# Kernel optimization log

Measured on AMD Instinct MI355X. Metric: run time of the kernel, lower is better.

Reference implementation:

```python
import jax, jax.numpy as jnp
import numpy as np


def setup_inputs() -> dict:
    key = jax.random.key(0)
    k1, k2 = jax.random.split(key)
    n, c, h, w = 32, 256, 64, 64
    x = jax.random.normal(k1, (n, c, h, w), dtype=jnp.float32)
    tau = jax.random.uniform(k2, (), dtype=jnp.float32)  # blend factor in (0,1)
    return {"x": x, "tau": tau, "topk_keep_num": 409}


def reference(x, tau, topk_keep_num):
    # x: [n, c, h, w]; keep top-k |x| entries over the flattened h*w axis per (n, c).
    n, c, h, w = x.shape
    hw = h * w
    if topk_keep_num == hw:
        return x
    xr = x.reshape(n, c, hw)
    # top-k indices by absolute value along last axis
    _, idx = jax.lax.top_k(jnp.abs(xr), topk_keep_num)  # idx: [n, c, k]
    # scatter ones at selected positions (torch.zeros_like(...).scatter_(2, idx, 1))
    bi = jnp.arange(n)[:, None, None]
    ci = jnp.arange(c)[None, :, None]
    mask = jnp.zeros_like(xr).at[bi, ci, idx].set(1.0)
    sparse_x = (mask * xr).reshape(n, c, h, w)
    # blend: sparse_x * tau + x * (1 - tau)  (tau == 1.0 reduces to sparse_x)
    return sparse_x * tau + x * (1.0 - tau)
```

## Files before the change

### kernel.cpp

```cpp
#include <hip/hip_runtime.h>
#include <hip/hip_bf16.h>

#define TPB 256
#define HW 4096

typedef unsigned int uint32;

template<int NB>
__device__ inline void find_crossing(uint32* hist, uint32* chunkSum, uint32 kk,
                                     uint32* sh_bin, uint32* sh_rank)
{
    const int tid = threadIdx.x;
    constexpr int CH = NB / TPB;
    uint32 s = 0;
#pragma unroll
    for (int j = 0; j < CH; ++j) s += hist[tid * CH + j];
    chunkSum[tid] = s;
    __syncthreads();
    if (tid < 64) {
        uint32 g = 0;
#pragma unroll
        for (int j = 0; j < 4; ++j) g += chunkSum[tid * 4 + j];
        uint32 suf = g;
#pragma unroll
        for (int d = 1; d < 64; d <<= 1) {
            uint32 v = __shfl_down(suf, d, 64);
            suf += (tid + d < 64) ? v : 0u;
        }
        unsigned long long m = __ballot(suf >= kk);
        int lstar = 63 - __clzll(m);
        uint32 cumAbove = (lstar < 63) ? __shfl(suf, lstar + 1, 64) : 0u;
        if (tid == lstar) {
            uint32 c = cumAbove;
            int bin = lstar * 4 * CH;
            uint32 rank = 1;
            bool done = false;
            for (int cc = lstar * 4 + 3; cc >= lstar * 4 && !done; --cc) {
                uint32 cs = chunkSum[cc];
                if (c + cs >= kk) {
                    for (int b = cc * CH + CH - 1; b >= cc * CH; --b) {
                        uint32 h = hist[b];
                        if (c + h >= kk) { bin = b; rank = kk - c; break; }
                        c += h;
                    }
                    done = true;
                } else {
                    c += cs;
                }
            }
            *sh_bin = (uint32)bin;
            *sh_rank = rank;
        }
    }
    __syncthreads();
}

__global__ void __launch_bounds__(TPB)
topk_blend_kernel(const float* __restrict__ x, const float* __restrict__ taup,
                  const int* __restrict__ kp, float* __restrict__ out, int nrows)
{
    __shared__ uint32 hist[2048];
    __shared__ uint32 chunkSum[TPB];
    __shared__ uint32 sh_bin, sh_rank, sh_cnt, sh_idxcut;

    const int tid = threadIdx.x;
    const int row = blockIdx.x;
    if (row >= nrows) return;

    const float4* xr  = reinterpret_cast<const float4*>(x + (size_t)row * HW);
    float4*       orw = reinterpret_cast<float4*>(out + (size_t)row * HW);

    float4 v[4];
#pragma unroll
    for (int j = 0; j < 4; ++j) v[j] = xr[tid + j * TPB];

    const uint32 K  = (uint32)(*kp);
    const float tau = *taup;

#pragma unroll
    for (int j = 0; j < 8; ++j) hist[tid + j * TPB] = 0;
    if (tid == 0) { sh_cnt = 0; sh_idxcut = 0xFFFFFFFFu; }
    __syncthreads();

    uint32 key[16];
#pragma unroll
    for (int j = 0; j < 4; ++j) {
        const float* pv = reinterpret_cast<const float*>(&v[j]);
#pragma unroll
        for (int l = 0; l < 4; ++l)
            key[j * 4 + l] = __float_as_uint(pv[l]) & 0x7fffffffu;
    }

#pragma unroll
    for (int e = 0; e < 16; ++e) atomicAdd(&hist[key[e] >> 20], 1u);
    __syncthreads();
    find_crossing<2048>(hist, chunkSum, K, &sh_bin, &sh_rank);
    const uint32 b1 = sh_bin;
    const uint32 k1 = sh_rank;

#pragma unroll
    for (int j = 0; j < 8; ++j) hist[tid + j * TPB] = 0;
    __syncthreads();
#pragma unroll
    for (int e = 0; e < 16; ++e)
        if ((key[e] >> 20) == b1) atomicAdd(&hist[(key[e] >> 9) & 2047u], 1u);
    __syncthreads();
    find_crossing<2048>(hist, chunkSum, k1, &sh_bin, &sh_rank);
    const uint32 b2 = sh_bin;
    const uint32 k2 = sh_rank;
    const uint32 p2 = (b1 << 11) | b2;

#pragma unroll
    for (int j = 0; j < 2; ++j) hist[tid + j * TPB] = 0;
    __syncthreads();
#pragma unroll
    for (int e = 0; e < 16; ++e)
        if ((key[e] >> 9) == p2) atomicAdd(&hist[key[e] & 511u], 1u);
    __syncthreads();
    find_crossing<512>(hist, chunkSum, k2, &sh_bin, &sh_rank);
    const uint32 b3  = sh_bin;
    const uint32 k3  = sh_rank;
    const uint32 ceq = hist[b3];
    const uint32 t   = (p2 << 9) | b3;

    uint32 idx_cut = 0xFFFFFFFFu;
    if (k3 < ceq) {
        uint32* tied = hist;
        __syncthreads();
#pragma unroll
        for (int e = 0; e < 16; ++e) {
            if (key[e] == t) {
                uint32 pos = atomicAdd(&sh_cnt, 1u);
                if (pos < 2048u) {
                    int j = e >> 2, l = e & 3;
                    tied[pos] = (uint32)(4 * (j * TPB + tid) + l);
                }
            }
        }
        __syncthreads();
        uint32 c2 = min(sh_cnt, 2048u);
        for (uint32 i = tid; i < c2; i += TPB) {
            uint32 my = tied[i];
            uint32 r = 0;
            for (uint32 jj = 0; jj < c2; ++jj) r += (tied[jj] < my) ? 1u : 0u;
            if (r == k3 - 1u) sh_idxcut = my;
        }
        __syncthreads();
        idx_cut = sh_idxcut;
    }

    const float om = 1.0f - tau;
#pragma unroll
    for (int j = 0; j < 4; ++j) {
        float4 o;
        const float* pv = reinterpret_cast<const float*>(&v[j]);
        float* po = reinterpret_cast<float*>(&o);
#pragma unroll
        for (int l = 0; l < 4; ++l) {
            int e = j * 4 + l;
            uint32 kb = key[e];
            uint32 eidx = (uint32)(4 * (j * TPB + tid) + l);
            bool keep = (kb > t) || (kb == t && eidx <= idx_cut);
            float xv = pv[l];
            po[l] = keep ? (xv * tau + xv * om) : (xv * om);
        }
        orw[tid + j * TPB] = o;
    }
}

extern "C" void kernel_launch(void* const* d_in, const int* in_sizes, int n_in,
                              void* d_out, int out_size, void* d_ws, size_t ws_size,
                              hipStream_t stream)
{
    (void)n_in; (void)out_size; (void)d_ws; (void)ws_size;
    const float* x   = (const float*)d_in[0];
    const float* tau = (const float*)d_in[1];
    const int*   kp  = (const int*)d_in[2];
    float*       out = (float*)d_out;
    const int nrows  = in_sizes[0] / HW;
    topk_blend_kernel<<<nrows, TPB, 0, stream>>>(x, tau, kp, out, nrows);
}
```

Measured before the change: 230.6 us.

## Replace three-pass radix select with one wide histogram plus candidate ranking

The three-level radix select (2048/2048/512 bins, each with its own find-crossing pass) becomes a single 4096-bin histogram on the top 12 bits of |x|. The crossing bin comes from a wave-level suffix scan plus a per-thread scan over 16 register-held bins. Elements in that bin are compacted into shared memory with ballot-based wave aggregation, then ranked brute-force on packed (low mantissa, reversed index) keys to find the exact cutoff. This removes two histogram rounds and several barriers, but the quadratic candidate ranking could get expensive if many values land in one bin.

```diff
diff --git a/kernel.cpp b/kernel.cpp
--- a/kernel.cpp
+++ b/kernel.cpp
@@ -3,165 +3,156 @@
 
 #define TPB 256
 #define HW 4096
+#define NB 4096
 
-typedef unsigned int uint32;
-
-template<int NB>
-__device__ inline void find_crossing(uint32* hist, uint32* chunkSum, uint32 kk,
-                                     uint32* sh_bin, uint32* sh_rank)
-{
-    const int tid = threadIdx.x;
-    constexpr int CH = NB / TPB;
-    uint32 s = 0;
-#pragma unroll
-    for (int j = 0; j < CH; ++j) s += hist[tid * CH + j];
-    chunkSum[tid] = s;
-    __syncthreads();
-    if (tid < 64) {
-        uint32 g = 0;
-#pragma unroll
-        for (int j = 0; j < 4; ++j) g += chunkSum[tid * 4 + j];
-        uint32 suf = g;
-#pragma unroll
-        for (int d = 1; d < 64; d <<= 1) {
-            uint32 v = __shfl_down(suf, d, 64);
-            suf += (tid + d < 64) ? v : 0u;
-        }
-        unsigned long long m = __ballot(suf >= kk);
-        int lstar = 63 - __clzll(m);
-        uint32 cumAbove = (lstar < 63) ? __shfl(suf, lstar + 1, 64) : 0u;
-        if (tid == lstar) {
-            uint32 c = cumAbove;
-            int bin = lstar * 4 * CH;
-            uint32 rank = 1;
-            bool done = false;
-            for (int cc = lstar * 4 + 3; cc >= lstar * 4 && !done; --cc) {
-                uint32 cs = chunkSum[cc];
-                if (c + cs >= kk) {
-                    for (int b = cc * CH + CH - 1; b >= cc * CH; --b) {
-                        uint32 h = hist[b];
-                        if (c + h >= kk) { bin = b; rank = kk - c; break; }
-                        c += h;
-                    }
-                    done = true;
-                } else {
-                    c += cs;
-                }
-            }
-            *sh_bin = (uint32)bin;
-            *sh_rank = rank;
-        }
-    }
-    __syncthreads();
-}
+typedef unsigned int u32;
+typedef unsigned long long u64;
 
 __global__ void __launch_bounds__(TPB)
 topk_blend_kernel(const float* __restrict__ x, const float* __restrict__ taup,
-                  const int* __restrict__ kp, float* __restrict__ out, int nrows)
+                  const int* __restrict__ kp, float* __restrict__ out)
 {
-    __shared__ uint32 hist[2048];
-    __shared__ uint32 chunkSum[TPB];
-    __shared__ uint32 sh_bin, sh_rank, sh_cnt, sh_idxcut;
+    __shared__ u32 hist[NB];
+    __shared__ u32 waveTot[4];
+    __shared__ u32 sh_b, sh_k1, sh_cnt, sh_pstar;
 
-    const int tid = threadIdx.x;
-    const int row = blockIdx.x;
-    if (row >= nrows) return;
+    const int tid  = threadIdx.x;
+    const int lane = tid & 63;
+    const int wv   = tid >> 6;
+    const int row  = blockIdx.x;
 
     const float4* xr  = reinterpret_cast<const float4*>(x + (size_t)row * HW);
     float4*       orw = reinterpret_cast<float4*>(out + (size_t)row * HW);
 
-    float4 v[4];
+    uint4* h4 = reinterpret_cast<uint4*>(hist);
+    const uint4 z4 = make_uint4(0u, 0u, 0u, 0u);
 #pragma unroll
-    for (int j = 0; j < 4; ++j) v[j] = xr[tid + j * TPB];
+    for (int j = 0; j < NB / 4 / TPB; ++j) h4[tid + j * TPB] = z4;
+    if (tid == 0) sh_cnt = 0;
 
-    const uint32 K  = (uint32)(*kp);
+    u32 r[16];
+#pragma unroll
+    for (int j = 0; j < 4; ++j) {
+        float4 v = xr[tid + j * TPB];
+        r[4 * j + 0] = __float_as_uint(v.x);
+        r[4 * j + 1] = __float_as_uint(v.y);
+        r[4 * j + 2] = __float_as_uint(v.z);
+        r[4 * j + 3] = __float_as_uint(v.w);
+    }
+    const u32  K   = (u32)(*kp);
     const float tau = *taup;
-
-#pragma unroll
-    for (int j = 0; j < 8; ++j) hist[tid + j * TPB] = 0;
-    if (tid == 0) { sh_cnt = 0; sh_idxcut = 0xFFFFFFFFu; }
     __syncthreads();
 
-    uint32 key[16];
+    if (K >= HW) {
 #pragma unroll
-    for (int j = 0; j < 4; ++j) {
-        const float* pv = reinterpret_cast<const float*>(&v[j]);
-#pragma unroll
-        for (int l = 0; l < 4; ++l)
-            key[j * 4 + l] = __float_as_uint(pv[l]) & 0x7fffffffu;
+        for (int j = 0; j < 4; ++j) {
+            float4 o;
+            o.x = __uint_as_float(r[4 * j + 0]);
+            o.y = __uint_as_float(r[4 * j + 1]);
+            o.z = __uint_as_float(r[4 * j + 2]);
+            o.w = __uint_as_float(r[4 * j + 3]);
+            orw[tid + j * TPB] = o;
+        }
+        return;
     }
 
 #pragma unroll
-    for (int e = 0; e < 16; ++e) atomicAdd(&hist[key[e] >> 20], 1u);
+    for (int e = 0; e < 16; ++e)
+        atomicAdd(&hist[(r[e] & 0x7fffffffu) >> 19], 1u);
     __syncthreads();
-    find_crossing<2048>(hist, chunkSum, K, &sh_bin, &sh_rank);
-    const uint32 b1 = sh_bin;
-    const uint32 k1 = sh_rank;
 
+    u32 hh[16];
+    {
+        uint4 a0 = h4[tid * 4 + 0], a1 = h4[tid * 4 + 1];
+        uint4 a2 = h4[tid * 4 + 2], a3 = h4[tid * 4 + 3];
+        hh[0]=a0.x; hh[1]=a0.y; hh[2]=a0.z;  hh[3]=a0.w;
+        hh[4]=a1.x; hh[5]=a1.y; hh[6]=a1.z;  hh[7]=a1.w;
+        hh[8]=a2.x; hh[9]=a2.y; hh[10]=a2.z; hh[11]=a2.w;
+        hh[12]=a3.x;hh[13]=a3.y;hh[14]=a3.z; hh[15]=a3.w;
+    }
+    u32 s = 0;
 #pragma unroll
-    for (int j = 0; j < 8; ++j) hist[tid + j * TPB] = 0;
+    for (int j = 0; j < 16; ++j) s += hh[j];
+
+    u32 suf = s;
+#pragma unroll
+    for (int d = 1; d < 64; d <<= 1) {
+        u32 t = __shfl_down(suf, d, 64);
+        if (lane + d < 64) suf += t;
+    }
+    if (lane == 0) waveTot[wv] = suf;
     __syncthreads();
+    u32 above = suf - s;
 #pragma unroll
-    for (int e = 0; e < 16; ++e)
-        if ((key[e] >> 20) == b1) atomicAdd(&hist[(key[e] >> 9) & 2047u], 1u);
-    __syncthreads();
-    find_crossing<2048>(hist, chunkSum, k1, &sh_bin, &sh_rank);
-    const uint32 b2 = sh_bin;
-    const uint32 k2 = sh_rank;
-    const uint32 p2 = (b1 << 11) | b2;
+    for (int w2 = 0; w2 < 4; ++w2)
+        if (w2 > wv) above += waveTot[w2];
 
+    if (above < K && above + s >= K) {
+        u32 c = above;
+        int fb = -1; u32 kk = 0;
 #pragma unroll
-    for (int j = 0; j < 2; ++j) hist[tid + j * TPB] = 0;
-    __syncthreads();
-#pragma unroll
-    for (int e = 0; e < 16; ++e)
-        if ((key[e] >> 9) == p2) atomicAdd(&hist[key[e] & 511u], 1u);
-    __syncthreads();
-    find_crossing<512>(hist, chunkSum, k2, &sh_bin, &sh_rank);
-    const uint32 b3  = sh_bin;
-    const uint32 k3  = sh_rank;
-    const uint32 ceq = hist[b3];
-    const uint32 t   = (p2 << 9) | b3;
-
-    uint32 idx_cut = 0xFFFFFFFFu;
-    if (k3 < ceq) {
-        uint32* tied = hist;
-        __syncthreads();
-#pragma unroll
-        for (int e = 0; e < 16; ++e) {
-            if (key[e] == t) {
-                uint32 pos = atomicAdd(&sh_cnt, 1u);
-                if (pos < 2048u) {
-                    int j = e >> 2, l = e & 3;
-                    tied[pos] = (uint32)(4 * (j * TPB + tid) + l);
-                }
+        for (int bi = 15; bi >= 0; --bi) {
+            u32 hb = hh[bi];
+            if (fb < 0) {
+                if (c + hb >= K) { fb = bi; kk = K - c; }
+                else c += hb;
             }
         }
-        __syncthreads();
-        uint32 c2 = min(sh_cnt, 2048u);
-        for (uint32 i = tid; i < c2; i += TPB) {
-            uint32 my = tied[i];
-            uint32 r = 0;
-            for (uint32 jj = 0; jj < c2; ++jj) r += (tied[jj] < my) ? 1u : 0u;
-            if (r == k3 - 1u) sh_idxcut = my;
+        sh_b  = (u32)(tid * 16 + fb);
+        sh_k1 = kk;
+    }
+    __syncthreads();
+
+    const u32 bstar = sh_b;
+    const u32 k1    = sh_k1;
+
+    u32* cand = hist;
+#pragma unroll
+    for (int e = 0; e < 16; ++e) {
+        u32 key = r[e] & 0x7fffffffu;
+        bool inb = ((key >> 19) == bstar);
+        u64 m = __ballot(inb);
+        if (m) {
+            int leader = (int)(__ffsll((long long)m) - 1);
+            u32 base = 0;
+            if (lane == leader) base = atomicAdd(&sh_cnt, (u32)__popcll(m));
+            base = __shfl(base, leader, 64);
+            if (inb) {
+                int j = e >> 2, l = e & 3;
+                u32 idx  = (u32)((((j * TPB + tid) << 2) | l));
+                u32 pack = ((key & 0x7ffffu) << 12) | (4095u - idx);
+                cand[base + (u32)__popcll(m & ((1ull << lane) - 1ull))] = pack;
+            }
         }
-        __syncthreads();
-        idx_cut = sh_idxcut;
     }
+    __syncthreads();
+
+    const u32 ceq = sh_cnt;
+    for (u32 i = tid; i < ceq; i += TPB) {
+        u32 p  = cand[i];
+        u32 rk = 0;
+        for (u32 j2 = 0; j2 < ceq; ++j2)
+            rk += (cand[j2] > p) ? 1u : 0u;
+        if (rk == k1 - 1u) sh_pstar = p;
+    }
+    __syncthreads();
+    const u32 pstar = sh_pstar;
 
     const float om = 1.0f - tau;
 #pragma unroll
     for (int j = 0; j < 4; ++j) {
         float4 o;
-        const float* pv = reinterpret_cast<const float*>(&v[j]);
         float* po = reinterpret_cast<float*>(&o);
 #pragma unroll
         for (int l = 0; l < 4; ++l) {
-            int e = j * 4 + l;
-            uint32 kb = key[e];
-            uint32 eidx = (uint32)(4 * (j * TPB + tid) + l);
-            bool keep = (kb > t) || (kb == t && eidx <= idx_cut);
-            float xv = pv[l];
+            int e = 4 * j + l;
+            u32 rb   = r[e];
+            u32 key  = rb & 0x7fffffffu;
+            u32 bin  = key >> 19;
+            u32 idx  = (u32)((((j * TPB + tid) << 2) | l));
+            u32 pack = ((key & 0x7ffffu) << 12) | (4095u - idx);
+            bool keep = (bin > bstar) || (bin == bstar && pack >= pstar);
+            float xv = __uint_as_float(rb);
             po[l] = keep ? (xv * tau + xv * om) : (xv * om);
         }
         orw[tid + j * TPB] = o;
@@ -178,5 +169,5 @@
     const int*   kp  = (const int*)d_in[2];
     float*       out = (float*)d_out;
     const int nrows  = in_sizes[0] / HW;
-    topk_blend_kernel<<<nrows, TPB, 0, stream>>>(x, tau, kp, out, nrows);
+    topk_blend_kernel<<<nrows, TPB, 0, stream>>>(x, tau, kp, out);
 }
```

Measured after the change: 232.3 us. About the same (+0.7%).
